# Kernel optimization log

Hardware: AMD Instinct MI355X
Metric: run time of the kernel (lower is better)

The kernel has to match this reference:

```python
import jax, jax.numpy as jnp
import numpy as np

D_MODEL, H, G, NPG = 2048, 256, 8, 512
B, N = 4, G * NPG


def _normalize(x, eps=1e-5):
    # F.normalize: x / max(||x||_2, eps) along last dim
    n = jnp.sqrt(jnp.sum(x * x, axis=-1, keepdims=True))
    return x / jnp.maximum(n, eps)


def _layernorm(x, g, b, eps=1e-5):
    mu = jnp.mean(x, axis=-1, keepdims=True)
    var = jnp.mean((x - mu) ** 2, axis=-1, keepdims=True)
    return (x - mu) * jax.lax.rsqrt(var + eps) * g + b


def setup_inputs() -> dict:
    key = jax.random.key(0)
    ks = jax.random.split(key, 12)
    s = 0.02
    return {
        "x": jax.random.normal(ks[0], (B, N, D_MODEL), jnp.float32),
        "M_prev": jax.random.normal(ks[1], (B, G, H, H), jnp.float32) * 0.1,
        "Wq": jax.random.normal(ks[2], (D_MODEL, H), jnp.float32) * s,
        "bq": jnp.zeros((H,), jnp.float32),
        "Wk": jax.random.normal(ks[3], (D_MODEL, H), jnp.float32) * s,
        "bk": jnp.zeros((H,), jnp.float32),
        "Wv": jax.random.normal(ks[4], (D_MODEL, H), jnp.float32) * s,
        "bv": jnp.zeros((H,), jnp.float32),
        "ln_g": jnp.ones((H,), jnp.float32),
        "ln_b": jnp.zeros((H,), jnp.float32),
        "Wo": jax.random.normal(ks[5], (H, D_MODEL), jnp.float32) * s,
        "bo": jnp.zeros((D_MODEL,), jnp.float32),
        "Wd": jax.random.normal(ks[6], (D_MODEL, 1), jnp.float32) * s,
        "bd": jnp.zeros((1,), jnp.float32),
        "timescale": jnp.linspace(-3.0, 8.0, G).reshape(1, G, 1).astype(jnp.float32),
    }


def reference(x, M_prev, Wq, bq, Wk, bk, Wv, bv, ln_g, ln_b, Wo, bo, Wd, bd, timescale):
    q = _normalize(x @ Wq + bq)                      # [B,N,H]
    k = _normalize(x @ Wk + bk)                      # [B,N,H]
    v = _layernorm(x @ Wv + bv, ln_g, ln_b)          # [B,N,H]

    BG = B * G
    M_f = M_prev.reshape(BG, H, H)
    k_f = k.reshape(BG, NPG, H)
    v_f = v.reshape(BG, NPG, H)
    q_f = q.reshape(BG, NPG, H)

    # v_pred = k @ M^T   [BG,NPG,H]
    v_pred = jnp.einsum('bnh,bmh->bnm', k_f, M_f)
    surprise = v_f - v_pred
    # delta_M = surprise^T @ k / NPG   [BG,H,H]
    delta_M = jnp.einsum('bnm,bnh->bmh', surprise, k_f) / NPG

    gamma = jax.nn.sigmoid(
        (x @ Wd + bd).reshape(B, G, NPG, 1).mean(axis=2) + timescale
    )[..., None]                                     # [B,G,1,1]

    M_next = jnp.clip(gamma * M_prev + delta_M.reshape(B, G, H, H), -10.0, 10.0)

    out_f = jnp.einsum('bnh,bmh->bnm', q_f, M_next.reshape(BG, H, H))  # [BG,NPG,H]
    out = out_f.reshape(B, N, H) @ Wo + bo
    return out, M_next
```

## Files before the change

kernel.cpp:

```cpp
#include <hip/hip_runtime.h>
#include <stdint.h>

typedef __bf16 bf16;
typedef bf16  bf16x4 __attribute__((ext_vector_type(4)));
typedef bf16  bf16x8 __attribute__((ext_vector_type(8)));
typedef float f32x4  __attribute__((ext_vector_type(4)));

__device__ __forceinline__ void gll16(const void* g, void* l) {
  __builtin_amdgcn_global_load_lds(
      (__attribute__((address_space(1))) void*)g,
      (__attribute__((address_space(3))) void*)l, 16, 0, 0);
}

__global__ __launch_bounds__(256) void k_prep(
    const float* __restrict__ Wq, const float* __restrict__ Wk, const float* __restrict__ Wv,
    const float* __restrict__ Wo, const float* __restrict__ Mp, const float* __restrict__ x,
    const float* __restrict__ Wd,
    bf16* __restrict__ Wt, bf16* __restrict__ WoT, bf16* __restrict__ Mb,
    bf16* __restrict__ xb, float* __restrict__ rowdot) {
  __shared__ float tle[32][33];
  const int id = blockIdx.x, t = threadIdx.x;
  if (id < 1536) {
    const float* src = id < 512 ? Wq : (id < 1024 ? Wk : Wv);
    bf16* dst = Wt + (size_t)(id / 512) * 256 * 2048;
    int lid = id & 511;
    int r0 = (lid >> 3) * 32, c0 = (lid & 7) * 32;
    int i = t >> 5, j = t & 31;
#pragma unroll
    for (int p = 0; p < 4; p++) tle[i + 8 * p][j] = src[(size_t)(r0 + i + 8 * p) * 256 + c0 + j];
    __syncthreads();
#pragma unroll
    for (int p = 0; p < 4; p++)
      dst[(size_t)(c0 + i + 8 * p) * 2048 + r0 + j] = (bf16)tle[j][i + 8 * p];
  } else if (id < 2048) {
    int lid = id - 1536;
    int r0 = (lid >> 6) * 32, c0 = (lid & 63) * 32;
    int i = t >> 5, j = t & 31;
#pragma unroll
    for (int p = 0; p < 4; p++) tle[i + 8 * p][j] = Wo[(size_t)(r0 + i + 8 * p) * 2048 + c0 + j];
    __syncthreads();
#pragma unroll
    for (int p = 0; p < 4; p++)
      WoT[(size_t)(c0 + i + 8 * p) * 256 + r0 + j] = (bf16)tle[j][i + 8 * p];
  } else if (id < 4096) {
    int i = (id - 2048) * 256 + t;
    f32x4 v = *(const f32x4*)(Mp + (size_t)i * 4);
    bf16x4 o; o[0] = (bf16)v[0]; o[1] = (bf16)v[1]; o[2] = (bf16)v[2]; o[3] = (bf16)v[3];
    *(bf16x4*)(Mb + (size_t)i * 4) = o;
  } else {
    const int lane = t & 63, w = t >> 6;
    const int row = (id - 4096) * 4 + w;
    const float* xp = x + (size_t)row * 2048;
    bf16* op = xb + (size_t)row * 2048;
    float dot = 0.f;
#pragma unroll
    for (int u = 0; u < 8; u++) {
      int off = u * 256 + lane * 4;
      f32x4 v  = *(const f32x4*)(xp + off);
      f32x4 wv = *(const f32x4*)(Wd + off);
      dot += v[0] * wv[0] + v[1] * wv[1] + v[2] * wv[2] + v[3] * wv[3];
      bf16x4 o; o[0] = (bf16)v[0]; o[1] = (bf16)v[1]; o[2] = (bf16)v[2]; o[3] = (bf16)v[3];
      *(bf16x4*)(op + off) = o;
    }
#pragma unroll
    for (int s = 32; s; s >>= 1) dot += __shfl_xor(dot, s);
    if (lane == 0) rowdot[row] = dot;
  }
}

__global__ __launch_bounds__(512) void k_qkv(const bf16* __restrict__ xb,
    const bf16* __restrict__ Wt,
    const float* __restrict__ bq, const float* __restrict__ bk, const float* __restrict__ bv,
    const float* __restrict__ lng, const float* __restrict__ lnb,
    bf16* __restrict__ qkvh) {
  __shared__ bf16 As[3][4096];
  __shared__ bf16 Bs[3][8192];
  __shared__ float red1[512], red2[512];
  const int t = threadIdx.x, lane = t & 63, w = t >> 6;
  const int sec = blockIdx.y;
  const int row0 = blockIdx.x * 128, n0 = sec * 256;
  const int wr = (w & 1) * 64, wc = (w >> 1) * 64;
  const int l15 = lane & 15, ql = lane >> 4;
  f32x4 acc[4][4] = {};

  auto STAGE = [&](int buf, int kt) {
    const int kb = kt * 32;
    { int r = t >> 2, gl = (t & 3) ^ ((r >> 1) & 3);
      gll16(xb + (size_t)(row0 + r) * 2048 + kb + gl * 8, &As[buf][(t & ~63) * 8]); }
#pragma unroll
    for (int i = 0; i < 2; i++) {
      int s = i * 512 + t;
      int r = s >> 2, gl = (s & 3) ^ ((r >> 1) & 3);
      gll16(Wt + (size_t)(n0 + r) * 2048 + kb + gl * 8, &Bs[buf][(i * 512 + (t & ~63)) * 8]);
    }
  };
  auto COMPUTE = [&](int buf) {
    bf16x8 af[4], bfv[4];
#pragma unroll
    for (int m = 0; m < 4; m++) {
      int ra = wr + m * 16 + l15;
      af[m] = *(const bf16x8*)&As[buf][ra * 32 + ((ql ^ ((ra >> 1) & 3)) << 3)];
    }
#pragma unroll
    for (int n = 0; n < 4; n++) {
      int rb = wc + n * 16 + l15;
      bfv[n] = *(const bf16x8*)&Bs[buf][rb * 32 + ((ql ^ ((rb >> 1) & 3)) << 3)];
    }
#pragma unroll
    for (int m = 0; m < 4; m++)
#pragma unroll
      for (int n = 0; n < 4; n++)
        acc[m][n] = __builtin_amdgcn_mfma_f32_16x16x32_bf16(af[m], bfv[n], acc[m][n], 0, 0, 0);
  };

  STAGE(0, 0);
  STAGE(1, 1);
  for (int tt = 0; tt < 64; ++tt) {
    if (tt < 62) {
      STAGE((tt + 2) % 3, tt + 2);
      asm volatile("s_waitcnt vmcnt(6)" ::: "memory");
    } else if (tt == 62) {
      asm volatile("s_waitcnt vmcnt(3)" ::: "memory");
    } else {
      asm volatile("s_waitcnt vmcnt(0)" ::: "memory");
    }
    __builtin_amdgcn_s_barrier();
    COMPUTE(tt % 3);
    __builtin_amdgcn_s_barrier();
  }

  __syncthreads();
  const float* bias = sec == 0 ? bq : (sec == 1 ? bk : bv);
#pragma unroll
  for (int m = 0; m < 4; m++)
#pragma unroll
    for (int j = 0; j < 4; j++) {
      float p1 = 0.f, p2 = 0.f;
#pragma unroll
      for (int n = 0; n < 4; n++) {
        float v = acc[m][n][j] + bias[wc + n * 16 + l15];
        p1 += v; p2 += v * v;
      }
#pragma unroll
      for (int mask = 8; mask; mask >>= 1) {
        p1 += __shfl_xor(p1, mask);
        p2 += __shfl_xor(p2, mask);
      }
      if (l15 == 0) {
        int rl = wr + m * 16 + ql * 4 + j;
        red1[rl * 4 + (w >> 1)] = p1;
        red2[rl * 4 + (w >> 1)] = p2;
      }
    }
  __syncthreads();
#pragma unroll
  for (int m = 0; m < 4; m++)
#pragma unroll
    for (int j = 0; j < 4; j++) {
      int rl = wr + m * 16 + ql * 4 + j;
      float s1 = red1[rl * 4] + red1[rl * 4 + 1] + red1[rl * 4 + 2] + red1[rl * 4 + 3];
      float s2 = red2[rl * 4] + red2[rl * 4 + 1] + red2[rl * 4 + 2] + red2[rl * 4 + 3];
      float sc = 1.f / fmaxf(sqrtf(s2), 1e-5f);
      float mu = s1 * (1.f / 256.f);
      float rs = rsqrtf(s2 * (1.f / 256.f) - mu * mu + 1e-5f);
#pragma unroll
      for (int n = 0; n < 4; n++) {
        int c = wc + n * 16 + l15;
        float v = acc[m][n][j] + bias[c];
        float o = sec < 2 ? v * sc : (v - mu) * rs * lng[c] + lnb[c];
        qkvh[(size_t)(row0 + rl) * 768 + n0 + c] = (bf16)o;
      }
    }
}

__global__ __launch_bounds__(256) void k_gamma(const float* __restrict__ rowdot,
    const float* __restrict__ bd, const float* __restrict__ ts, float* __restrict__ gamma) {
  __shared__ float red[256];
  const int t = threadIdx.x, bg = blockIdx.x;
  red[t] = rowdot[bg * 512 + t] + rowdot[bg * 512 + 256 + t];
  __syncthreads();
  if (t < 64) {
    float s = red[t] + red[t + 64] + red[t + 128] + red[t + 192];
#pragma unroll
    for (int sh = 32; sh; sh >>= 1) s += __shfl_down(s, sh);
    if (t == 0) gamma[bg] = 1.f / (1.f + expf(-(s * (1.f / 512.f) + bd[0] + ts[bg & 7])));
  }
}

__global__ __launch_bounds__(512) void k_qM(const bf16* __restrict__ qkvh,
    const bf16* __restrict__ M, bf16* __restrict__ out, int sec, int dosub) {
  __shared__ bf16 Al[3][4096];
  __shared__ bf16 Bl[3][4096];
  const int t = threadIdx.x, lane = t & 63, w = t >> 6;
  const int bg = blockIdx.x, nb = blockIdx.y, mb = blockIdx.z;
  const int row0 = bg * 512 + nb * 128, m0 = mb * 128;
  const int wrow = (w & 1) * 64, wcol = (w >> 1) * 32;
  const int l15 = lane & 15, ql = lane >> 4;
  f32x4 acc[4][2] = {};

  auto STAGE = [&](int buf, int kt) {
    const int kb = kt * 32;
    int r = t >> 2, gl = (t & 3) ^ ((r >> 1) & 3);
    gll16(qkvh + (size_t)(row0 + r) * 768 + sec + kb + gl * 8, &Al[buf][(t & ~63) * 8]);
    gll16(M + (size_t)bg * 65536 + (size_t)(m0 + r) * 256 + kb + gl * 8, &Bl[buf][(t & ~63) * 8]);
  };
  auto COMPUTE = [&](int buf) {
    bf16x8 af[4], bfv[2];
#pragma unroll
    for (int m = 0; m < 4; m++) {
      int ra = wrow + m * 16 + l15;
      af[m] = *(const bf16x8*)&Al[buf][ra * 32 + ((ql ^ ((ra >> 1) & 3)) << 3)];
    }
#pragma unroll
    for (int n = 0; n < 2; n++) {
      int rb = wcol + n * 16 + l15;
      bfv[n] = *(const bf16x8*)&Bl[buf][rb * 32 + ((ql ^ ((rb >> 1) & 3)) << 3)];
    }
#pragma unroll
    for (int m = 0; m < 4; m++)
#pragma unroll
      for (int n = 0; n < 2; n++)
        acc[m][n] = __builtin_amdgcn_mfma_f32_16x16x32_bf16(af[m], bfv[n], acc[m][n], 0, 0, 0);
  };

  STAGE(0, 0);
  STAGE(1, 1);
  for (int tt = 0; tt < 8; ++tt) {
    if (tt < 6) {
      STAGE((tt + 2) % 3, tt + 2);
      asm volatile("s_waitcnt vmcnt(4)" ::: "memory");
    } else if (tt == 6) {
      asm volatile("s_waitcnt vmcnt(2)" ::: "memory");
    } else {
      asm volatile("s_waitcnt vmcnt(0)" ::: "memory");
    }
    __builtin_amdgcn_s_barrier();
    COMPUTE(tt % 3);
    __builtin_amdgcn_s_barrier();
  }
#pragma unroll
  for (int m = 0; m < 4; m++)
#pragma unroll
    for (int n = 0; n < 2; n++)
#pragma unroll
      for (int j = 0; j < 4; j++) {
        int gr = row0 + wrow + m * 16 + ql * 4 + j;
        int c = m0 + wcol + n * 16 + l15;
        float val = acc[m][n][j];
        if (dosub) val = (float)qkvh[(size_t)gr * 768 + 512 + c] - val;
        out[(size_t)gr * 256 + c] = (bf16)val;
      }
}

__global__ __launch_bounds__(512) void k_deltaM(const bf16* __restrict__ s,
    const bf16* __restrict__ qkvh, const float* __restrict__ Mp,
    const float* __restrict__ gamma, float* __restrict__ Mnext, bf16* __restrict__ Mnb) {
  __shared__ bf16 Sl[2][8192];
  __shared__ bf16 Kl[2][4096];
  const int t = threadIdx.x, lane = t & 63, w = t >> 6;
  const int bg = blockIdx.x;
  const int m0 = blockIdx.y * 128, h0 = blockIdx.z * 64;
  const int wm = (w & 3) * 32, wh = (w >> 2) * 32;
  const int l15 = lane & 15, g8 = (lane >> 4) * 8;
  const int nl = t & 63, cj = t >> 6;
  f32x4 acc[2][2] = {};

  bf16x8 vs0, vs1, vk;
  auto LOADREGS = [&](int kb) {
    vs0 = *(const bf16x8*)(s + (size_t)(bg * 512 + kb + nl) * 256 + m0 + cj * 8);
    vs1 = *(const bf16x8*)(s + (size_t)(bg * 512 + kb + nl) * 256 + m0 + 64 + cj * 8);
    vk  = *(const bf16x8*)(qkvh + (size_t)(bg * 512 + kb + nl) * 768 + 256 + h0 + cj * 8);
  };
  auto DSWRITE = [&](int buf) {
#pragma unroll
    for (int e = 0; e < 8; e++) {
      int m = cj * 8 + e;
      Sl[buf][m * 64 + (nl ^ ((m & 7) * 8))] = vs0[e];
      int m2 = m + 64;
      Sl[buf][m2 * 64 + (nl ^ ((m2 & 7) * 8))] = vs1[e];
      Kl[buf][m * 64 + (nl ^ ((m & 7) * 8))] = vk[e];
    }
  };

  LOADREGS(0);
  DSWRITE(0);
  __syncthreads();
  int cur = 0;
  for (int it = 0; it < 8; ++it) {
    if (it < 7) LOADREGS((it + 1) * 64);
#pragma unroll
    for (int kk = 0; kk < 64; kk += 32) {
      bf16x8 af[2], bfv[2];
#pragma unroll
      for (int m = 0; m < 2; m++) {
        int ml = wm + m * 16 + l15;
        af[m] = *(const bf16x8*)&Sl[cur][ml * 64 + ((kk + g8) ^ ((ml & 7) * 8))];
      }
#pragma unroll
      for (int n = 0; n < 2; n++) {
        int hl = wh + n * 16 + l15;
        bfv[n] = *(const bf16x8*)&Kl[cur][hl * 64 + ((kk + g8) ^ ((hl & 7) * 8))];
      }
#pragma unroll
      for (int m = 0; m < 2; m++)
#pragma unroll
        for (int n = 0; n < 2; n++)
          acc[m][n] = __builtin_amdgcn_mfma_f32_16x16x32_bf16(af[m], bfv[n], acc[m][n], 0, 0, 0);
    }
    if (it < 7) DSWRITE(cur ^ 1);
    __syncthreads();
    cur ^= 1;
  }
  const float gm = gamma[bg];
#pragma unroll
  for (int m = 0; m < 2; m++)
#pragma unroll
    for (int n = 0; n < 2; n++)
#pragma unroll
      for (int j = 0; j < 4; j++) {
        int mg = m0 + wm + m * 16 + (lane >> 4) * 4 + j;
        int hg = h0 + wh + n * 16 + l15;
        size_t idx = (size_t)bg * 65536 + (size_t)mg * 256 + hg;
        float val = gm * Mp[idx] + acc[m][n][j] * (1.f / 512.f);
        val = fminf(10.f, fmaxf(-10.f, val));
        Mnext[idx] = val;
        Mnb[idx] = (bf16)val;
      }
}

__global__ __launch_bounds__(512) void k_out(const bf16* __restrict__ outf,
    const bf16* __restrict__ WoT, const float* __restrict__ bo, float* __restrict__ out) {
  __shared__ bf16 As[3][4096];
  __shared__ bf16 Bs[3][8192];
  const int t = threadIdx.x, lane = t & 63, w = t >> 6;
  const int row0 = blockIdx.x * 128, n0 = blockIdx.y * 256;
  const int wr = (w & 1) * 64, wc = (w >> 1) * 64;
  const int l15 = lane & 15, ql = lane >> 4;
  f32x4 acc[4][4] = {};

  auto STAGE = [&](int buf, int kt) {
    const int kb = kt * 32;
    { int r = t >> 2, gl = (t & 3) ^ ((r >> 1) & 3);
      gll16(outf + (size_t)(row0 + r) * 256 + kb + gl * 8, &As[buf][(t & ~63) * 8]); }
#pragma unroll
    for (int i = 0; i < 2; i++) {
      int s = i * 512 + t;
      int r = s >> 2, gl = (s & 3) ^ ((r >> 1) & 3);
      gll16(WoT + (size_t)(n0 + r) * 256 + kb + gl * 8, &Bs[buf][(i * 512 + (t & ~63)) * 8]);
    }
  };
  auto COMPUTE = [&](int buf) {
    bf16x8 af[4], bfv[4];
#pragma unroll
    for (int m = 0; m < 4; m++) {
      int ra = wr + m * 16 + l15;
      af[m] = *(const bf16x8*)&As[buf][ra * 32 + ((ql ^ ((ra >> 1) & 3)) << 3)];
    }
#pragma unroll
    for (int n = 0; n < 4; n++) {
      int rb = wc + n * 16 + l15;
      bfv[n] = *(const bf16x8*)&Bs[buf][rb * 32 + ((ql ^ ((rb >> 1) & 3)) << 3)];
    }
#pragma unroll
    for (int m = 0; m < 4; m++)
#pragma unroll
      for (int n = 0; n < 4; n++)
        acc[m][n] = __builtin_amdgcn_mfma_f32_16x16x32_bf16(af[m], bfv[n], acc[m][n], 0, 0, 0);
  };

  STAGE(0, 0);
  STAGE(1, 1);
  for (int tt = 0; tt < 8; ++tt) {
    if (tt < 6) {
      STAGE((tt + 2) % 3, tt + 2);
      asm volatile("s_waitcnt vmcnt(6)" ::: "memory");
    } else if (tt == 6) {
      asm volatile("s_waitcnt vmcnt(3)" ::: "memory");
    } else {
      asm volatile("s_waitcnt vmcnt(0)" ::: "memory");
    }
    __builtin_amdgcn_s_barrier();
    COMPUTE(tt % 3);
    __builtin_amdgcn_s_barrier();
  }
#pragma unroll
  for (int m = 0; m < 4; m++)
#pragma unroll
    for (int n = 0; n < 4; n++)
#pragma unroll
      for (int j = 0; j < 4; j++) {
        int r = row0 + wr + m * 16 + ql * 4 + j;
        int c = n0 + wc + n * 16 + l15;
        out[(size_t)r * 2048 + c] = acc[m][n][j] + bo[c];
      }
}

extern "C" void kernel_launch(void* const* d_in, const int* in_sizes, int n_in,
                              void* d_out, int out_size, void* d_ws, size_t ws_size,
                              hipStream_t stream) {
  const float* x   = (const float*)d_in[0];
  const float* Mp  = (const float*)d_in[1];
  const float* Wq  = (const float*)d_in[2];
  const float* bq  = (const float*)d_in[3];
  const float* Wk  = (const float*)d_in[4];
  const float* bk  = (const float*)d_in[5];
  const float* Wv  = (const float*)d_in[6];
  const float* bv  = (const float*)d_in[7];
  const float* lng = (const float*)d_in[8];
  const float* lnb = (const float*)d_in[9];
  const float* Wo  = (const float*)d_in[10];
  const float* bo  = (const float*)d_in[11];
  const float* Wd  = (const float*)d_in[12];
  const float* bd  = (const float*)d_in[13];
  const float* ts  = (const float*)d_in[14];

  char* ws = (char*)d_ws;
  bf16*  Wt     = (bf16*)(ws);
  bf16*  WoT    = (bf16*)(ws + 3145728);
  bf16*  Mb     = (bf16*)(ws + 4194304);
  bf16*  qkvh   = (bf16*)(ws + 8388608);
  bf16*  sbuf   = (bf16*)(ws + 33554432);
  bf16*  Mnb    = (bf16*)(ws + 41943040);
  bf16*  outf   = (bf16*)(ws + 46137344);
  float* rowdot = (float*)(ws + 54525952);
  float* gamma  = (float*)(ws + 54591488);

  float* out   = (float*)d_out;
  float* Mnext = (float*)d_out + 33554432;
  bf16*  xb    = (bf16*)d_out;

  dim3 b256(256), b512(512);
  k_prep<<<dim3(8192),       b256, 0, stream>>>(Wq, Wk, Wv, Wo, Mp, x, Wd, Wt, WoT, Mb, xb, rowdot);
  k_qkv<<<dim3(128, 3),      b512, 0, stream>>>(xb, Wt, bq, bk, bv, lng, lnb, qkvh);
  k_gamma<<<dim3(32),        b256, 0, stream>>>(rowdot, bd, ts, gamma);
  k_qM<<<dim3(32, 4, 2),     b512, 0, stream>>>(qkvh, Mb, sbuf, 256, 1);
  k_deltaM<<<dim3(32, 2, 4), b512, 0, stream>>>(sbuf, qkvh, Mp, gamma, Mnext, Mnb);
  k_qM<<<dim3(32, 4, 2),     b512, 0, stream>>>(qkvh, Mnb, outf, 0, 0);
  k_out<<<dim3(128, 8),      b512, 0, stream>>>(outf, WoT, bo, out);
}
```

Measured before the change: 203.2 us.

## Enlarge QKV GEMM tile to 256 rows with 4-stage split A/B pipeline

```diff
diff --git a/kernel.cpp b/kernel.cpp
--- a/kernel.cpp
+++ b/kernel.cpp
@@ -73,66 +73,91 @@
     const float* __restrict__ bq, const float* __restrict__ bk, const float* __restrict__ bv,
     const float* __restrict__ lng, const float* __restrict__ lnb,
     bf16* __restrict__ qkvh) {
-  __shared__ bf16 As[3][4096];
-  __shared__ bf16 Bs[3][8192];
-  __shared__ float red1[512], red2[512];
+  __shared__ bf16 As[4][8192];
+  __shared__ bf16 Bs[4][8192];
   const int t = threadIdx.x, lane = t & 63, w = t >> 6;
   const int sec = blockIdx.y;
-  const int row0 = blockIdx.x * 128, n0 = sec * 256;
-  const int wr = (w & 1) * 64, wc = (w >> 1) * 64;
+  const int row0 = blockIdx.x * 256, n0 = sec * 256;
+  const int wr = (w & 1) * 128, wc = (w >> 1) * 64;
   const int l15 = lane & 15, ql = lane >> 4;
-  f32x4 acc[4][4] = {};
-
-  auto STAGE = [&](int buf, int kt) {
+  f32x4 acc[8][4] = {};
+
+  auto STAGE_A = [&](int slot, int kt) {
     const int kb = kt * 32;
-    { int r = t >> 2, gl = (t & 3) ^ ((r >> 1) & 3);
-      gll16(xb + (size_t)(row0 + r) * 2048 + kb + gl * 8, &As[buf][(t & ~63) * 8]); }
 #pragma unroll
     for (int i = 0; i < 2; i++) {
       int s = i * 512 + t;
       int r = s >> 2, gl = (s & 3) ^ ((r >> 1) & 3);
-      gll16(Wt + (size_t)(n0 + r) * 2048 + kb + gl * 8, &Bs[buf][(i * 512 + (t & ~63)) * 8]);
-    }
-  };
-  auto COMPUTE = [&](int buf) {
-    bf16x8 af[4], bfv[4];
-#pragma unroll
-    for (int m = 0; m < 4; m++) {
-      int ra = wr + m * 16 + l15;
-      af[m] = *(const bf16x8*)&As[buf][ra * 32 + ((ql ^ ((ra >> 1) & 3)) << 3)];
-    }
+      gll16(xb + (size_t)(row0 + r) * 2048 + kb + gl * 8, &As[slot][(i * 512 + (t & ~63)) * 8]);
+    }
+  };
+  auto STAGE_B = [&](int slot, int kt) {
+    const int kb = kt * 32;
+#pragma unroll
+    for (int i = 0; i < 2; i++) {
+      int s = i * 512 + t;
+      int r = s >> 2, gl = (s & 3) ^ ((r >> 1) & 3);
+      gll16(Wt + (size_t)(n0 + r) * 2048 + kb + gl * 8, &Bs[slot][(i * 512 + (t & ~63)) * 8]);
+    }
+  };
+
+  STAGE_A(0, 0); STAGE_B(0, 0);
+  STAGE_A(1, 1); STAGE_B(1, 1);
+  STAGE_A(2, 2); STAGE_B(2, 2);
+
+  for (int tt = 0; tt < 64; ++tt) {
+    const int slot = tt & 3;
+    asm volatile("s_waitcnt vmcnt(8)" ::: "memory");
+    __builtin_amdgcn_s_barrier();
+
+    bf16x8 bfv[4];
+    if (tt <= 60) STAGE_A((tt + 3) & 3, tt + 3);
 #pragma unroll
     for (int n = 0; n < 4; n++) {
       int rb = wc + n * 16 + l15;
-      bfv[n] = *(const bf16x8*)&Bs[buf][rb * 32 + ((ql ^ ((rb >> 1) & 3)) << 3)];
-    }
-#pragma unroll
-    for (int m = 0; m < 4; m++)
-#pragma unroll
-      for (int n = 0; n < 4; n++)
-        acc[m][n] = __builtin_amdgcn_mfma_f32_16x16x32_bf16(af[m], bfv[n], acc[m][n], 0, 0, 0);
-  };
-
-  STAGE(0, 0);
-  STAGE(1, 1);
-  for (int tt = 0; tt < 64; ++tt) {
-    if (tt < 62) {
-      STAGE((tt + 2) % 3, tt + 2);
-      asm volatile("s_waitcnt vmcnt(6)" ::: "memory");
-    } else if (tt == 62) {
-      asm volatile("s_waitcnt vmcnt(3)" ::: "memory");
-    } else {
-      asm volatile("s_waitcnt vmcnt(0)" ::: "memory");
-    }
-    __builtin_amdgcn_s_barrier();
-    COMPUTE(tt % 3);
-    __builtin_amdgcn_s_barrier();
+      bfv[n] = *(const bf16x8*)&Bs[slot][rb * 32 + ((ql ^ ((rb >> 1) & 3)) << 3)];
+    }
+    {
+      bf16x8 af[4];
+#pragma unroll
+      for (int m = 0; m < 4; m++) {
+        int ra = wr + m * 16 + l15;
+        af[m] = *(const bf16x8*)&As[slot][ra * 32 + ((ql ^ ((ra >> 1) & 3)) << 3)];
+      }
+      __builtin_amdgcn_s_setprio(1);
+#pragma unroll
+      for (int m = 0; m < 4; m++)
+#pragma unroll
+        for (int n = 0; n < 4; n++)
+          acc[m][n] = __builtin_amdgcn_mfma_f32_16x16x32_bf16(af[m], bfv[n], acc[m][n], 0, 0, 0);
+      __builtin_amdgcn_s_setprio(0);
+    }
+    __builtin_amdgcn_s_barrier();
+
+    if (tt <= 60) STAGE_B((tt + 3) & 3, tt + 3);
+    {
+      bf16x8 af[4];
+#pragma unroll
+      for (int m = 0; m < 4; m++) {
+        int ra = wr + 64 + m * 16 + l15;
+        af[m] = *(const bf16x8*)&As[slot][ra * 32 + ((ql ^ ((ra >> 1) & 3)) << 3)];
+      }
+      __builtin_amdgcn_s_setprio(1);
+#pragma unroll
+      for (int m = 0; m < 4; m++)
+#pragma unroll
+        for (int n = 0; n < 4; n++)
+          acc[4 + m][n] = __builtin_amdgcn_mfma_f32_16x16x32_bf16(af[m], bfv[n], acc[4 + m][n], 0, 0, 0);
+      __builtin_amdgcn_s_setprio(0);
+    }
   }
 
   __syncthreads();
+  float* red1 = (float*)&As[0][0];
+  float* red2 = (float*)&As[2][0];
   const float* bias = sec == 0 ? bq : (sec == 1 ? bk : bv);
 #pragma unroll
-  for (int m = 0; m < 4; m++)
+  for (int m = 0; m < 8; m++)
 #pragma unroll
     for (int j = 0; j < 4; j++) {
       float p1 = 0.f, p2 = 0.f;
@@ -154,7 +179,7 @@
     }
   __syncthreads();
 #pragma unroll
-  for (int m = 0; m < 4; m++)
+  for (int m = 0; m < 8; m++)
 #pragma unroll
     for (int j = 0; j < 4; j++) {
       int rl = wr + m * 16 + ql * 4 + j;
@@ -431,7 +456,7 @@
 
   dim3 b256(256), b512(512);
   k_prep<<<dim3(8192),       b256, 0, stream>>>(Wq, Wk, Wv, Wo, Mp, x, Wd, Wt, WoT, Mb, xb, rowdot);
-  k_qkv<<<dim3(128, 3),      b512, 0, stream>>>(xb, Wt, bq, bk, bv, lng, lnb, qkvh);
+  k_qkv<<<dim3(64, 3),       b512, 0, stream>>>(xb, Wt, bq, bk, bv, lng, lnb, qkvh);
   k_gamma<<<dim3(32),        b256, 0, stream>>>(rowdot, bd, ts, gamma);
   k_qM<<<dim3(32, 4, 2),     b512, 0, stream>>>(qkvh, Mb, sbuf, 256, 1);
   k_deltaM<<<dim3(32, 2, 4), b512, 0, stream>>>(sbuf, qkvh, Mp, gamma, Mnext, Mnb);
```

New measurement: 221.2 us. 1.09x slower.
